# Kernel optimization log

Hardware: AMD Instinct MI355X
Metric: run time of the kernel (lower is better)

The kernel has to match this reference:

```python
import jax, jax.numpy as jnp
import numpy as np

COMMITMENT_COST = 0.25
EPS = 1e-10


def setup_inputs() -> dict:
    key = jax.random.key(0)
    k1, k2 = jax.random.split(key)
    z = jax.random.normal(k1, (8, 2048, 512), dtype=jnp.float32)
    # codebook ~ small uniform init in torch; small normal is fine for a numeric reference
    codebook = jax.random.normal(k2, (4096, 512), dtype=jnp.float32) * 0.02
    return {"z": z, "codebook": codebook}


def reference(z, codebook):
    B, S, D = z.shape
    K = codebook.shape[0]
    flat_z = z.reshape(-1, D)  # [N, D]
    distances = (
        jnp.sum(flat_z * flat_z, axis=1, keepdims=True)
        + jnp.sum(codebook * codebook, axis=1)
        - 2.0 * flat_z @ codebook.T
    )
    encoding_indices = jnp.argmin(distances, axis=1)  # [N] int
    z_q = codebook[encoding_indices].reshape(z.shape)  # gather lookup
    # commitment loss (z_q detached)
    commitment_loss = jnp.mean((z - jax.lax.stop_gradient(z_q)) ** 2)
    loss = COMMITMENT_COST * commitment_loss
    # straight-through estimator
    z_q_st = z + jax.lax.stop_gradient(z_q - z)
    # perplexity from codebook usage histogram
    N = flat_z.shape[0]
    counts = jnp.zeros((K,), dtype=jnp.float32).at[encoding_indices].add(1.0)
    avg_probs = counts / N
    perplexity = jnp.exp(-jnp.sum(avg_probs * jnp.log(avg_probs + EPS)))
    encoding_indices = encoding_indices.reshape(B, S)
    return (z_q_st, loss, encoding_indices, perplexity)
```

## Files before the change

### kernel.cpp

```cpp
#include <hip/hip_runtime.h>
#include <hip/hip_fp16.h>
#include <stdint.h>

#define B_  8
#define S_  2048
#define D_  512
#define K_  4096
#define N_  (B_ * S_)
#define NCB (K_ / 128)
#define NKB32 (D_ / 32)
#define MARGIN 0.014f

typedef _Float16 half8  __attribute__((ext_vector_type(8)));
typedef float    floatx4 __attribute__((ext_vector_type(4)));

#define OFF_PK   0
#define OFF_EN   (OFF_PK + (size_t)N_ * NCB * 8)
#define OFF_ZN   (OFF_EN + K_ * 4)
#define OFF_CNT  (OFF_ZN + N_ * 4)
#define OFF_BL   (OFF_CNT + K_ * 4)
#define OFF_ZH   (OFF_BL + 4096 * 4)
#define OFF_EH   (OFF_ZH + (size_t)N_ * D_ * 2)

__device__ __forceinline__ uint32_t umin32(uint32_t a, uint32_t b) { return a < b ? a : b; }
__device__ __forceinline__ uint32_t umax32(uint32_t a, uint32_t b) { return a > b ? a : b; }
__device__ __forceinline__ bool lexlt(float va, int ia, float vb, int ib) {
    return va < vb || (va == vb && ia < ib);
}

__device__ __forceinline__ void load_lds16(const _Float16* g, _Float16* l) {
    __builtin_amdgcn_global_load_lds(
        (const __attribute__((address_space(1))) unsigned int*)(uintptr_t)g,
        (__attribute__((address_space(3))) unsigned int*)(uintptr_t)l,
        16, 0, 0);
}

__global__ __launch_bounds__(256)
void vq_prep_kernel(const float* __restrict__ z, const float* __restrict__ cb,
                    _Float16* __restrict__ zh, _Float16* __restrict__ eh,
                    float* __restrict__ znorm, float* __restrict__ enorm,
                    int* __restrict__ counts) {
    const int t = threadIdx.x;
    if (blockIdx.x < 16) counts[blockIdx.x * 256 + t] = 0;

    const size_t u = (size_t)blockIdx.x * 256 + t;
    const int c   = (int)(u & 63);
    const int row = (int)(u >> 6);
    const bool isZ = row < N_;
    const int n = isZ ? row : row - N_;
    const float* r = (isZ ? z : cb) + (size_t)n * D_;

    float s = 0.f;
    for (int j = c; j < D_; j += 64) { float v = r[j]; s += v * v; }
    #pragma unroll
    for (int m = 1; m < 64; m <<= 1) s += __shfl_xor(s, m, 64);
    if (c == 0) { if (isZ) znorm[n] = s; else enorm[n] = s; }

    const float scale = isZ ? 1.0f : 64.0f;
    const float4 v0 = *(const float4*)(r + c * 8);
    const float4 v1 = *(const float4*)(r + c * 8 + 4);
    float a[8] = {v0.x, v0.y, v0.z, v0.w, v1.x, v1.y, v1.z, v1.w};
    half8 h;
    #pragma unroll
    for (int j = 0; j < 8; j++) h[j] = (_Float16)(a[j] * scale);
    const int kb = c >> 2, qd = c & 3;
    const int sw = qd ^ ((n >> 1) & 3);
    const size_t rows = isZ ? (size_t)N_ : (size_t)K_;
    const size_t off = (size_t)kb * rows * 32 + (size_t)n * 32 + (size_t)(sw << 3);
    *(half8*)((isZ ? zh : eh) + off) = h;
}

__global__ __launch_bounds__(256, 4)
void vq_dist_kernel(const _Float16* __restrict__ zh, const _Float16* __restrict__ eh,
                    const float* __restrict__ enorm, const float* __restrict__ znorm,
                    uint2* __restrict__ pK) {
    __shared__ _Float16 sA[2][4096];
    __shared__ float sE[128], sZn[128];
    __shared__ uint2 cK[2][128];

    const int t  = threadIdx.x;
    const int c0 = blockIdx.x * 128;
    const int m0 = blockIdx.y * 128;

    if (t < 128) { sE[t] = enorm[c0 + t]; sZn[t] = znorm[m0 + t]; }

    const int lane = t & 63, wid = t >> 6;
    const int wr = wid & 1, wc = wid >> 1;
    const int qd = lane >> 4, nl = lane & 15;
    const int sw8 = (qd ^ ((nl >> 1) & 3)) << 3;

    const _Float16* gsrc = zh + (size_t)m0 * 32 + (size_t)(wid * 2) * 512 + (size_t)lane * 8;
    const size_t strideA = (size_t)N_ * 32;
    const size_t strideB = (size_t)K_ * 32;
    const _Float16* bptr = eh + (size_t)c0 * 32 + (size_t)((wc * 64 + nl) * 32 + sw8);
    const int aoff = (wr * 64 + nl) * 32 + sw8;

    floatx4 acc[4][4];
    #pragma unroll
    for (int i = 0; i < 4; i++)
        #pragma unroll
        for (int j = 0; j < 4; j++) acc[i][j] = (floatx4)0.f;

    #pragma unroll
    for (int g = 0; g < 2; g++)
        load_lds16(gsrc + g * 512, sA[0] + wid * 2 * 512 + g * 512);

    for (int kb = 0; kb < NKB32; kb++) {
        __syncthreads();

        half8 b_h[4];
        #pragma unroll
        for (int s = 0; s < 4; s++)
            b_h[s] = *(const half8*)(bptr + s * 512);
        if (kb + 1 < NKB32) {
            const _Float16* gk = gsrc + (size_t)(kb + 1) * strideA;
            _Float16* ld = sA[(kb + 1) & 1] + wid * 2 * 512;
            #pragma unroll
            for (int g = 0; g < 2; g++)
                load_lds16(gk + g * 512, ld + g * 512);
        }
        const _Float16* ah = sA[kb & 1] + aoff;
        half8 a_h[4];
        #pragma unroll
        for (int s = 0; s < 4; s++)
            a_h[s] = *(const half8*)(ah + s * 512);
        #pragma unroll
        for (int i = 0; i < 4; i++)
            #pragma unroll
            for (int j = 0; j < 4; j++)
                acc[i][j] = __builtin_amdgcn_mfma_f32_16x16x32_f16(a_h[i], b_h[j], acc[i][j], 0, 0, 0);
        bptr += strideB;
    }

    uint32_t colc[4]; float se4[4];
    #pragma unroll
    for (int sn = 0; sn < 4; sn++) {
        const int cl = wc * 64 + sn * 16 + nl;
        colc[sn] = (uint32_t)cl;
        se4[sn]  = sE[cl];
    }
    #pragma unroll
    for (int sm = 0; sm < 4; sm++) {
        #pragma unroll
        for (int reg = 0; reg < 4; reg++) {
            const int rm = wr * 64 + sm * 16 + qd * 4 + reg;
            const float zn = sZn[rm];
            uint32_t k0 = 0xFFFFFFFFu, k1 = 0xFFFFFFFFu;
            #pragma unroll
            for (int sn = 0; sn < 4; sn++) {
                const float v = fmaf(acc[sm][sn][reg], -0.03125f, zn + se4[sn]);
                const uint32_t key = (__float_as_uint(v) & 0xFFFFFF80u) | colc[sn];
                const uint32_t t1 = umax32(k0, key);
                k1 = umin32(k1, t1);
                k0 = umin32(k0, key);
            }
            #pragma unroll
            for (int msk = 1; msk <= 8; msk <<= 1) {
                const uint32_t o0 = (uint32_t)__shfl_xor((int)k0, msk, 64);
                const uint32_t o1 = (uint32_t)__shfl_xor((int)k1, msk, 64);
                const uint32_t n0 = umin32(k0, o0);
                k1 = umin32(umax32(k0, o0), umin32(k1, o1));
                k0 = n0;
            }
            if (nl == 0) { cK[wc][rm].x = k0; cK[wc][rm].y = k1; }
        }
    }
    __syncthreads();
    if (t < 128) {
        const uint2 a = cK[0][t], b = cK[1][t];
        uint2 r;
        r.x = umin32(a.x, b.x);
        r.y = umin32(umax32(a.x, b.x), umin32(a.y, b.y));
        pK[(size_t)(m0 + t) * NCB + blockIdx.x] = r;
    }
}

__global__ __launch_bounds__(256)
void vq_gather_kernel(const float* __restrict__ z, const float* __restrict__ cb,
                      const float* __restrict__ znorm, const float* __restrict__ enorm,
                      const uint2* __restrict__ pK,
                      float* __restrict__ out_zq, float* __restrict__ out_idx,
                      int* __restrict__ counts, float* __restrict__ blockLoss) {
    const int lane = threadIdx.x & 63, wid = threadIdx.x >> 6;
    const int m = blockIdx.x * 4 + wid;

    uint32_t k0 = 0xFFFFFFFFu, k1 = 0xFFFFFFFFu;
    if (lane < NCB) {
        const uint2 kk = pK[(size_t)m * NCB + lane];
        k0 = kk.x; k1 = kk.y;
    }
    uint32_t g = k0;
    #pragma unroll
    for (int msk = 1; msk < 64; msk <<= 1) {
        const uint32_t o = (uint32_t)__shfl_xor((int)g, msk, 64);
        g = umin32(g, o);
    }
    const float gvf = __uint_as_float(g & 0xFFFFFF80u) + MARGIN;
    const bool f0 = (lane < NCB) && (__uint_as_float(k0 & 0xFFFFFF80u) <= gvf);
    const bool f1 = (lane < NCB) && (__uint_as_float(k1 & 0xFFFFFF80u) <= gvf);
    const unsigned long long b0 = __ballot(f0), b1 = __ballot(f1);
    int idx;
    if (__popcll(b0) + __popcll(b1) <= 1) {
        const unsigned long long bw = __ballot(k0 == g);
        idx = (int)__builtin_ctzll(bw) * 128 + (int)(g & 0x7Fu);
    } else {
        const float zn = znorm[m];
        const float* zrow = z + (size_t)m * D_;
        float bestd = 1e30f; int besti = 0x7fffffff;
        #pragma unroll
        for (int slot = 0; slot < 2; slot++) {
            unsigned long long bm = slot ? b1 : b0;
            while (bm) {
                const int l = (int)__builtin_ctzll(bm); bm &= bm - 1;
                const uint32_t kx = (uint32_t)__shfl((int)(slot ? k1 : k0), l, 64);
                const int cand = l * 128 + (int)(kx & 0x7Fu);
                const float* crow = cb + (size_t)cand * D_;
                float s = 0.f;
                #pragma unroll
                for (int j = 0; j < 8; j++)
                    s += zrow[lane * 8 + j] * crow[lane * 8 + j];
                #pragma unroll
                for (int msk = 1; msk < 64; msk <<= 1) s += __shfl_xor(s, msk, 64);
                const float d = (zn + enorm[cand]) - 2.0f * s;
                if (lexlt(d, cand, bestd, besti)) { bestd = d; besti = cand; }
            }
        }
        idx = besti;
    }

    const float4* qrow  = (const float4*)(cb + (size_t)idx * D_);
    const float4* zrow4 = (const float4*)(z + (size_t)m * D_);
    float4*       orow  = (float4*)(out_zq + (size_t)m * D_);
    float lsum = 0.f;
    #pragma unroll
    for (int i = 0; i < 2; i++) {
        const int j = lane + i * 64;
        const float4 q  = qrow[j];
        const float4 zv = zrow4[j];
        float4 o;
        o.x = zv.x + (q.x - zv.x); o.y = zv.y + (q.y - zv.y);
        o.z = zv.z + (q.z - zv.z); o.w = zv.w + (q.w - zv.w);
        orow[j] = o;
        const float dx = zv.x - q.x, dy = zv.y - q.y, dz = zv.z - q.z, dw = zv.w - q.w;
        lsum += dx * dx + dy * dy + dz * dz + dw * dw;
    }
    #pragma unroll
    for (int msk = 1; msk < 64; msk <<= 1) lsum += __shfl_xor(lsum, msk, 64);

    if (lane == 0) {
        out_idx[m] = (float)idx;
        atomicAdd(&counts[idx], 1);
    }
    __shared__ float wl[4];
    if (lane == 0) wl[wid] = lsum;
    __syncthreads();
    if (threadIdx.x == 0) blockLoss[blockIdx.x] = wl[0] + wl[1] + wl[2] + wl[3];
}

__global__ void vq_final_kernel(const int* __restrict__ counts,
                                const float* __restrict__ blockLoss,
                                float* __restrict__ out_loss, float* __restrict__ out_ppl) {
    __shared__ float sl[256], se[256];
    const int t = threadIdx.x;
    float ls = 0.f, es = 0.f;
    for (int i = t; i < N_ / 4; i += 256) ls += blockLoss[i];
    for (int k = t; k < K_; k += 256) {
        const float p = (float)counts[k] / (float)N_;
        es += p * logf(p + 1e-10f);
    }
    sl[t] = ls; se[t] = es;
    __syncthreads();
    for (int s = 128; s > 0; s >>= 1) {
        if (t < s) { sl[t] += sl[t + s]; se[t] += se[t + s]; }
        __syncthreads();
    }
    if (t == 0) {
        out_loss[0] = 0.25f * (sl[0] / (float)((size_t)N_ * D_));
        out_ppl[0]  = expf(-se[0]);
    }
}

extern "C" void kernel_launch(void* const* d_in, const int* in_sizes, int n_in,
                              void* d_out, int out_size, void* d_ws, size_t ws_size,
                              hipStream_t stream) {
    const float* z  = (const float*)d_in[0];
    const float* cb = (const float*)d_in[1];
    float* out = (float*)d_out;

    char* ws = (char*)d_ws;
    uint2*    pK        = (uint2*)   (ws + OFF_PK);
    float*    enorm     = (float*)   (ws + OFF_EN);
    float*    znorm     = (float*)   (ws + OFF_ZN);
    int*      counts    = (int*)     (ws + OFF_CNT);
    float*    blockLoss = (float*)   (ws + OFF_BL);
    _Float16* zh        = (_Float16*)(ws + OFF_ZH);
    _Float16* eh        = (_Float16*)(ws + OFF_EH);

    float* out_zq   = out;
    float* out_loss = out + (size_t)N_ * D_;
    float* out_idx  = out_loss + 1;
    float* out_ppl  = out_idx + N_;

    vq_prep_kernel<<<(N_ + K_) * 64 / 256, 256, 0, stream>>>(z, cb, zh, eh,
                                                             znorm, enorm, counts);

    dim3 grid(K_ / 128, N_ / 128);
    vq_dist_kernel<<<grid, 256, 0, stream>>>(zh, eh, enorm, znorm, pK);

    vq_gather_kernel<<<N_ / 4, 256, 0, stream>>>(z, cb, znorm, enorm, pK,
                                                 out_zq, out_idx, counts, blockLoss);

    vq_final_kernel<<<1, 256, 0, stream>>>(counts, blockLoss, out_loss, out_ppl);
}
```

Before: 205.2 us.

## Enlarge distance GEMM tile to 256x256 with 4-stage LDS pipeline for both operands

The distance kernel moves from 128x128 tiles with 256 threads to 256x256 tiles with 512 threads. Both the z and codebook fragments are now staged into LDS through a 4-deep ring of async global-to-LDS loads, using explicit vmcnt waits, raw barriers and MFMA priority boosts. Each wave computes 128x64 outputs in two half-steps, which raises reuse per loaded byte and overlaps loads with MFMA work. The cost is more registers and LDS per block, fewer blocks in the grid, and hand-tuned waitcnt logic that is fragile. The partial argmin output keeps its layout, written as two 128-column halves per block.

```diff
diff --git a/kernel.cpp b/kernel.cpp
--- a/kernel.cpp
+++ b/kernel.cpp
@@ -35,6 +35,9 @@
         16, 0, 0);
 }
 
+#define BARR() do { asm volatile("" ::: "memory"); __builtin_amdgcn_s_barrier(); \
+                    asm volatile("" ::: "memory"); } while (0)
+
 __global__ __launch_bounds__(256)
 void vq_prep_kernel(const float* __restrict__ z, const float* __restrict__ cb,
                     _Float16* __restrict__ zh, _Float16* __restrict__ eh,
@@ -70,84 +73,115 @@
     *(half8*)((isZ ? zh : eh) + off) = h;
 }
 
-__global__ __launch_bounds__(256, 4)
+__global__ __launch_bounds__(512, 2)
 void vq_dist_kernel(const _Float16* __restrict__ zh, const _Float16* __restrict__ eh,
                     const float* __restrict__ enorm, const float* __restrict__ znorm,
                     uint2* __restrict__ pK) {
-    __shared__ _Float16 sA[2][4096];
-    __shared__ float sE[128], sZn[128];
-    __shared__ uint2 cK[2][128];
+    __shared__ __align__(16) _Float16 sA[4][256 * 32];
+    __shared__ __align__(16) _Float16 sB[4][256 * 32];
 
     const int t  = threadIdx.x;
-    const int c0 = blockIdx.x * 128;
-    const int m0 = blockIdx.y * 128;
-
-    if (t < 128) { sE[t] = enorm[c0 + t]; sZn[t] = znorm[m0 + t]; }
-
+    const int c0 = blockIdx.x * 256;
+    const int m0 = blockIdx.y * 256;
     const int lane = t & 63, wid = t >> 6;
     const int wr = wid & 1, wc = wid >> 1;
     const int qd = lane >> 4, nl = lane & 15;
     const int sw8 = (qd ^ ((nl >> 1) & 3)) << 3;
 
-    const _Float16* gsrc = zh + (size_t)m0 * 32 + (size_t)(wid * 2) * 512 + (size_t)lane * 8;
     const size_t strideA = (size_t)N_ * 32;
     const size_t strideB = (size_t)K_ * 32;
-    const _Float16* bptr = eh + (size_t)c0 * 32 + (size_t)((wc * 64 + nl) * 32 + sw8);
-    const int aoff = (wr * 64 + nl) * 32 + sw8;
-
-    floatx4 acc[4][4];
-    #pragma unroll
-    for (int i = 0; i < 4; i++)
+    const _Float16* gA = zh + (size_t)m0 * 32;
+    const _Float16* gB = eh + (size_t)c0 * 32;
+    const size_t uo0 = (size_t)t * 8;
+    const size_t uo1 = (size_t)(512 + t) * 8;
+    const int lb0 = wid * 512;
+    const int lb1 = 4096 + wid * 512;
+
+    auto stageA = [&](int kb) {
+        const _Float16* g = gA + (size_t)kb * strideA;
+        _Float16* l = &sA[kb & 3][0];
+        load_lds16(g + uo0, l + lb0);
+        load_lds16(g + uo1, l + lb1);
+    };
+    auto stageB = [&](int kb) {
+        const _Float16* g = gB + (size_t)kb * strideB;
+        _Float16* l = &sB[kb & 3][0];
+        load_lds16(g + uo0, l + lb0);
+        load_lds16(g + uo1, l + lb1);
+    };
+
+    const int aBase = (wr * 128 + nl) * 32 + sw8;
+    const int bBase = (wc * 64 + nl) * 32 + sw8;
+
+    floatx4 acc[8][4];
+    #pragma unroll
+    for (int i = 0; i < 8; i++)
         #pragma unroll
         for (int j = 0; j < 4; j++) acc[i][j] = (floatx4)0.f;
 
-    #pragma unroll
-    for (int g = 0; g < 2; g++)
-        load_lds16(gsrc + g * 512, sA[0] + wid * 2 * 512 + g * 512);
-
-    for (int kb = 0; kb < NKB32; kb++) {
-        __syncthreads();
-
-        half8 b_h[4];
-        #pragma unroll
-        for (int s = 0; s < 4; s++)
-            b_h[s] = *(const half8*)(bptr + s * 512);
-        if (kb + 1 < NKB32) {
-            const _Float16* gk = gsrc + (size_t)(kb + 1) * strideA;
-            _Float16* ld = sA[(kb + 1) & 1] + wid * 2 * 512;
+    stageA(0); stageB(0);
+    stageA(1); stageB(1);
+    stageA(2); stageB(2);
+    asm volatile("s_waitcnt vmcnt(8)" ::: "memory");
+    BARR();
+
+    #pragma unroll
+    for (int s = 0; s < 16; ++s) {
+        const int slot = s & 3;
+        half8 b_h[4], a_h[4];
+        #pragma unroll
+        for (int j = 0; j < 4; ++j)
+            b_h[j] = *(const half8*)(&sB[slot][0] + bBase + j * 512);
+        #pragma unroll
+        for (int i = 0; i < 4; ++i)
+            a_h[i] = *(const half8*)(&sA[slot][0] + aBase + i * 512);
+        if (s < 13) stageA(s + 3);
+        BARR();
+        __builtin_amdgcn_s_setprio(1);
+        #pragma unroll
+        for (int i = 0; i < 4; ++i)
             #pragma unroll
-            for (int g = 0; g < 2; g++)
-                load_lds16(gk + g * 512, ld + g * 512);
-        }
-        const _Float16* ah = sA[kb & 1] + aoff;
-        half8 a_h[4];
-        #pragma unroll
-        for (int s = 0; s < 4; s++)
-            a_h[s] = *(const half8*)(ah + s * 512);
-        #pragma unroll
-        for (int i = 0; i < 4; i++)
+            for (int j = 0; j < 4; ++j)
+                acc[i][j] = __builtin_amdgcn_mfma_f32_16x16x32_f16(a_h[i], b_h[j], acc[i][j], 0, 0, 0);
+        __builtin_amdgcn_s_setprio(0);
+        BARR();
+        #pragma unroll
+        for (int i = 0; i < 4; ++i)
+            a_h[i] = *(const half8*)(&sA[slot][0] + aBase + 2048 + i * 512);
+        if (s < 13) stageB(s + 3);
+        BARR();
+        __builtin_amdgcn_s_setprio(1);
+        #pragma unroll
+        for (int i = 0; i < 4; ++i)
             #pragma unroll
-            for (int j = 0; j < 4; j++)
-                acc[i][j] = __builtin_amdgcn_mfma_f32_16x16x32_f16(a_h[i], b_h[j], acc[i][j], 0, 0, 0);
-        bptr += strideB;
-    }
+            for (int j = 0; j < 4; ++j)
+                acc[4 + i][j] = __builtin_amdgcn_mfma_f32_16x16x32_f16(a_h[i], b_h[j], acc[4 + i][j], 0, 0, 0);
+        __builtin_amdgcn_s_setprio(0);
+        if (s < 13)       { asm volatile("s_waitcnt vmcnt(8)" ::: "memory"); }
+        else if (s == 13) { asm volatile("s_waitcnt vmcnt(4)" ::: "memory"); }
+        else if (s == 14) { asm volatile("s_waitcnt vmcnt(0)" ::: "memory"); }
+        BARR();
+    }
+
+    uint2* cK = (uint2*)(&sA[0][0]);
 
     uint32_t colc[4]; float se4[4];
-    #pragma unroll
-    for (int sn = 0; sn < 4; sn++) {
-        const int cl = wc * 64 + sn * 16 + nl;
+    const int colbase = (wc & 1) * 64;
+    #pragma unroll
+    for (int sn = 0; sn < 4; ++sn) {
+        const int cl = colbase + sn * 16 + nl;
         colc[sn] = (uint32_t)cl;
-        se4[sn]  = sE[cl];
-    }
-    #pragma unroll
-    for (int sm = 0; sm < 4; sm++) {
-        #pragma unroll
-        for (int reg = 0; reg < 4; reg++) {
-            const int rm = wr * 64 + sm * 16 + qd * 4 + reg;
-            const float zn = sZn[rm];
+        se4[sn]  = enorm[c0 + wc * 64 + sn * 16 + nl];
+    }
+    #pragma unroll
+    for (int sm = 0; sm < 8; ++sm) {
+        #pragma unroll
+        for (int reg = 0; reg < 4; ++reg) {
+            const int rm = wr * 128 + sm * 16 + qd * 4 + reg;
+            const float zn = znorm[m0 + rm];
             uint32_t k0 = 0xFFFFFFFFu, k1 = 0xFFFFFFFFu;
             #pragma unroll
-            for (int sn = 0; sn < 4; sn++) {
+            for (int sn = 0; sn < 4; ++sn) {
                 const float v = fmaf(acc[sm][sn][reg], -0.03125f, zn + se4[sn]);
                 const uint32_t key = (__float_as_uint(v) & 0xFFFFFF80u) | colc[sn];
                 const uint32_t t1 = umax32(k0, key);
@@ -162,16 +196,18 @@
                 k1 = umin32(umax32(k0, o0), umin32(k1, o1));
                 k0 = n0;
             }
-            if (nl == 0) { cK[wc][rm].x = k0; cK[wc][rm].y = k1; }
+            if (nl == 0) { cK[wc * 256 + rm].x = k0; cK[wc * 256 + rm].y = k1; }
         }
     }
     __syncthreads();
-    if (t < 128) {
-        const uint2 a = cK[0][t], b = cK[1][t];
+    {
+        const int row = t & 255, b = t >> 8;
+        const uint2 a = cK[(b * 2) * 256 + row];
+        const uint2 c = cK[(b * 2 + 1) * 256 + row];
         uint2 r;
-        r.x = umin32(a.x, b.x);
-        r.y = umin32(umax32(a.x, b.x), umin32(a.y, b.y));
-        pK[(size_t)(m0 + t) * NCB + blockIdx.x] = r;
+        r.x = umin32(a.x, c.x);
+        r.y = umin32(umax32(a.x, c.x), umin32(a.y, c.y));
+        pK[(size_t)(m0 + row) * NCB + blockIdx.x * 2 + b] = r;
     }
 }
 
@@ -304,8 +340,8 @@
     vq_prep_kernel<<<(N_ + K_) * 64 / 256, 256, 0, stream>>>(z, cb, zh, eh,
                                                              znorm, enorm, counts);
 
-    dim3 grid(K_ / 128, N_ / 128);
-    vq_dist_kernel<<<grid, 256, 0, stream>>>(zh, eh, enorm, znorm, pK);
+    dim3 grid(K_ / 256, N_ / 256);
+    vq_dist_kernel<<<grid, 512, 0, stream>>>(zh, eh, enorm, znorm, pK);
 
     vq_gather_kernel<<<N_ / 4, 256, 0, stream>>>(z, cb, znorm, enorm, pK,
                                                  out_zq, out_idx, counts, blockLoss);
```

Result: slower. 217.3 us (+5.9%).

## Stage codebook tiles through LDS and fold final reduction into gather kernel

Applied to the files above, without the earlier changes.

The distance GEMM now loads the codebook (B) tile into double-buffered LDS with async global-to-LDS copies alongside the z tile, instead of each wave reading B fragments straight from global memory. The separate single-block final kernel is removed. The last gather block to finish, found with an atomic done-counter and thread fences, computes the loss and perplexity. This cuts redundant global traffic for B and one kernel launch, at the cost of twice the LDS per block, which may reduce occupancy, and an extra atomic in every gather block.

```diff
diff --git a/kernel.cpp b/kernel.cpp
--- a/kernel.cpp
+++ b/kernel.cpp
@@ -19,7 +19,8 @@
 #define OFF_ZN   (OFF_EN + K_ * 4)
 #define OFF_CNT  (OFF_ZN + N_ * 4)
 #define OFF_BL   (OFF_CNT + K_ * 4)
-#define OFF_ZH   (OFF_BL + 4096 * 4)
+#define OFF_DC   (OFF_BL + 4096 * 4)
+#define OFF_ZH   (OFF_DC + 64)
 #define OFF_EH   (OFF_ZH + (size_t)N_ * D_ * 2)
 
 __device__ __forceinline__ uint32_t umin32(uint32_t a, uint32_t b) { return a < b ? a : b; }
@@ -39,9 +40,10 @@
 void vq_prep_kernel(const float* __restrict__ z, const float* __restrict__ cb,
                     _Float16* __restrict__ zh, _Float16* __restrict__ eh,
                     float* __restrict__ znorm, float* __restrict__ enorm,
-                    int* __restrict__ counts) {
+                    int* __restrict__ counts, int* __restrict__ doneCnt) {
     const int t = threadIdx.x;
     if (blockIdx.x < 16) counts[blockIdx.x * 256 + t] = 0;
+    if (blockIdx.x == 16 && t == 0) doneCnt[0] = 0;
 
     const size_t u = (size_t)blockIdx.x * 256 + t;
     const int c   = (int)(u & 63);
@@ -74,7 +76,8 @@
 void vq_dist_kernel(const _Float16* __restrict__ zh, const _Float16* __restrict__ eh,
                     const float* __restrict__ enorm, const float* __restrict__ znorm,
                     uint2* __restrict__ pK) {
-    __shared__ _Float16 sA[2][4096];
+    __shared__ __align__(16) _Float16 sA[2][4096];
+    __shared__ __align__(16) _Float16 sB[2][4096];
     __shared__ float sE[128], sZn[128];
     __shared__ uint2 cK[2][128];
 
@@ -89,11 +92,13 @@
     const int qd = lane >> 4, nl = lane & 15;
     const int sw8 = (qd ^ ((nl >> 1) & 3)) << 3;
 
-    const _Float16* gsrc = zh + (size_t)m0 * 32 + (size_t)(wid * 2) * 512 + (size_t)lane * 8;
     const size_t strideA = (size_t)N_ * 32;
     const size_t strideB = (size_t)K_ * 32;
-    const _Float16* bptr = eh + (size_t)c0 * 32 + (size_t)((wc * 64 + nl) * 32 + sw8);
+    const _Float16* gA = zh + (size_t)m0 * 32 + (size_t)t * 8;
+    const _Float16* gB = eh + (size_t)c0 * 32 + (size_t)t * 8;
+
     const int aoff = (wr * 64 + nl) * 32 + sw8;
+    const int boff = (wc * 64 + nl) * 32 + sw8;
 
     floatx4 acc[4][4];
     #pragma unroll
@@ -101,24 +106,28 @@
         #pragma unroll
         for (int j = 0; j < 4; j++) acc[i][j] = (floatx4)0.f;
 
-    #pragma unroll
-    for (int g = 0; g < 2; g++)
-        load_lds16(gsrc + g * 512, sA[0] + wid * 2 * 512 + g * 512);
+    auto stage = [&](int kb) {
+        const _Float16* ga = gA + (size_t)kb * strideA;
+        const _Float16* gb = gB + (size_t)kb * strideB;
+        _Float16* la = sA[kb & 1] + t * 8;
+        _Float16* lb = sB[kb & 1] + t * 8;
+        load_lds16(ga, la);
+        load_lds16(ga + 2048, la + 2048);
+        load_lds16(gb, lb);
+        load_lds16(gb + 2048, lb + 2048);
+    };
+
+    stage(0);
 
     for (int kb = 0; kb < NKB32; kb++) {
         __syncthreads();
-
+        if (kb + 1 < NKB32) stage(kb + 1);
+
+        const _Float16* bh = sB[kb & 1] + boff;
         half8 b_h[4];
         #pragma unroll
         for (int s = 0; s < 4; s++)
-            b_h[s] = *(const half8*)(bptr + s * 512);
-        if (kb + 1 < NKB32) {
-            const _Float16* gk = gsrc + (size_t)(kb + 1) * strideA;
-            _Float16* ld = sA[(kb + 1) & 1] + wid * 2 * 512;
-            #pragma unroll
-            for (int g = 0; g < 2; g++)
-                load_lds16(gk + g * 512, ld + g * 512);
-        }
+            b_h[s] = *(const half8*)(bh + s * 512);
         const _Float16* ah = sA[kb & 1] + aoff;
         half8 a_h[4];
         #pragma unroll
@@ -129,7 +138,6 @@
             #pragma unroll
             for (int j = 0; j < 4; j++)
                 acc[i][j] = __builtin_amdgcn_mfma_f32_16x16x32_f16(a_h[i], b_h[j], acc[i][j], 0, 0, 0);
-        bptr += strideB;
     }
 
     uint32_t colc[4]; float se4[4];
@@ -180,7 +188,9 @@
                       const float* __restrict__ znorm, const float* __restrict__ enorm,
                       const uint2* __restrict__ pK,
                       float* __restrict__ out_zq, float* __restrict__ out_idx,
-                      int* __restrict__ counts, float* __restrict__ blockLoss) {
+                      int* __restrict__ counts, float* __restrict__ blockLoss,
+                      int* __restrict__ doneCnt,
+                      float* __restrict__ out_loss, float* __restrict__ out_ppl) {
     const int lane = threadIdx.x & 63, wid = threadIdx.x >> 6;
     const int m = blockIdx.x * 4 + wid;
 
@@ -255,28 +265,31 @@
     if (lane == 0) wl[wid] = lsum;
     __syncthreads();
     if (threadIdx.x == 0) blockLoss[blockIdx.x] = wl[0] + wl[1] + wl[2] + wl[3];
-}
-
-__global__ void vq_final_kernel(const int* __restrict__ counts,
-                                const float* __restrict__ blockLoss,
-                                float* __restrict__ out_loss, float* __restrict__ out_ppl) {
-    __shared__ float sl[256], se[256];
-    const int t = threadIdx.x;
-    float ls = 0.f, es = 0.f;
-    for (int i = t; i < N_ / 4; i += 256) ls += blockLoss[i];
-    for (int k = t; k < K_; k += 256) {
-        const float p = (float)counts[k] / (float)N_;
-        es += p * logf(p + 1e-10f);
-    }
-    sl[t] = ls; se[t] = es;
+
+    __shared__ int sLast;
+    __threadfence();
+    if (threadIdx.x == 0) sLast = (atomicAdd(doneCnt, 1) == (N_ / 4) - 1) ? 1 : 0;
     __syncthreads();
-    for (int s = 128; s > 0; s >>= 1) {
-        if (t < s) { sl[t] += sl[t + s]; se[t] += se[t + s]; }
+    if (sLast) {
+        __threadfence();
+        __shared__ float sl[256], se[256];
+        const int tt = threadIdx.x;
+        float ls = 0.f, es = 0.f;
+        for (int i = tt; i < N_ / 4; i += 256) ls += blockLoss[i];
+        for (int k = tt; k < K_; k += 256) {
+            const float p = (float)counts[k] / (float)N_;
+            es += p * logf(p + 1e-10f);
+        }
+        sl[tt] = ls; se[tt] = es;
         __syncthreads();
-    }
-    if (t == 0) {
-        out_loss[0] = 0.25f * (sl[0] / (float)((size_t)N_ * D_));
-        out_ppl[0]  = expf(-se[0]);
+        for (int s = 128; s > 0; s >>= 1) {
+            if (tt < s) { sl[tt] += sl[tt + s]; se[tt] += se[tt + s]; }
+            __syncthreads();
+        }
+        if (tt == 0) {
+            out_loss[0] = 0.25f * (sl[0] / (float)((size_t)N_ * D_));
+            out_ppl[0]  = expf(-se[0]);
+        }
     }
 }
 
@@ -293,6 +306,7 @@
     float*    znorm     = (float*)   (ws + OFF_ZN);
     int*      counts    = (int*)     (ws + OFF_CNT);
     float*    blockLoss = (float*)   (ws + OFF_BL);
+    int*      doneCnt   = (int*)     (ws + OFF_DC);
     _Float16* zh        = (_Float16*)(ws + OFF_ZH);
     _Float16* eh        = (_Float16*)(ws + OFF_EH);
 
@@ -302,13 +316,12 @@
     float* out_ppl  = out_idx + N_;
 
     vq_prep_kernel<<<(N_ + K_) * 64 / 256, 256, 0, stream>>>(z, cb, zh, eh,
-                                                             znorm, enorm, counts);
+                                                             znorm, enorm, counts, doneCnt);
 
     dim3 grid(K_ / 128, N_ / 128);
     vq_dist_kernel<<<grid, 256, 0, stream>>>(zh, eh, enorm, znorm, pK);
 
     vq_gather_kernel<<<N_ / 4, 256, 0, stream>>>(z, cb, znorm, enorm, pK,
-                                                 out_zq, out_idx, counts, blockLoss);
-
-    vq_final_kernel<<<1, 256, 0, stream>>>(counts, blockLoss, out_loss, out_ppl);
-}
+                                                 out_zq, out_idx, counts, blockLoss,
+                                                 doneCnt, out_loss, out_ppl);
+}
```

Measured after the change: 703.8 us. +243.0%, slower.

## Give each wave a private LDS A tile with two-stage prefetch and no block barriers

Applied to the files above, without the earlier changes.

Each wave now stages its own 64-row A slice into a private double-buffered LDS region, prefetching two k-steps ahead. The per-iteration __syncthreads is replaced by explicit vmcnt/lgkmcnt waits, removing block-wide synchronization from the main loop. The cost is duplicated A loads across the two waves that share a row half, plus twice the LDS footprint. Correctness now depends on the hand-coded wait counts matching the number of outstanding loads.

```diff
diff --git a/kernel.cpp b/kernel.cpp
--- a/kernel.cpp
+++ b/kernel.cpp
@@ -74,7 +74,7 @@
 void vq_dist_kernel(const _Float16* __restrict__ zh, const _Float16* __restrict__ eh,
                     const float* __restrict__ enorm, const float* __restrict__ znorm,
                     uint2* __restrict__ pK) {
-    __shared__ _Float16 sA[2][4096];
+    __shared__ __align__(16) _Float16 sAw[4][2][2048];
     __shared__ float sE[128], sZn[128];
     __shared__ uint2 cK[2][128];
 
@@ -89,11 +89,11 @@
     const int qd = lane >> 4, nl = lane & 15;
     const int sw8 = (qd ^ ((nl >> 1) & 3)) << 3;
 
-    const _Float16* gsrc = zh + (size_t)m0 * 32 + (size_t)(wid * 2) * 512 + (size_t)lane * 8;
     const size_t strideA = (size_t)N_ * 32;
     const size_t strideB = (size_t)K_ * 32;
+    const _Float16* gA = zh + (size_t)(m0 + wr * 64) * 32 + (size_t)lane * 8;
     const _Float16* bptr = eh + (size_t)c0 * 32 + (size_t)((wc * 64 + nl) * 32 + sw8);
-    const int aoff = (wr * 64 + nl) * 32 + sw8;
+    const int aoff = nl * 32 + sw8;
 
     floatx4 acc[4][4];
     #pragma unroll
@@ -101,36 +101,44 @@
         #pragma unroll
         for (int j = 0; j < 4; j++) acc[i][j] = (floatx4)0.f;
 
-    #pragma unroll
-    for (int g = 0; g < 2; g++)
-        load_lds16(gsrc + g * 512, sA[0] + wid * 2 * 512 + g * 512);
-
+    auto stage = [&](int kb) {
+        const _Float16* g = gA + (size_t)kb * strideA;
+        _Float16* l = &sAw[wid][kb & 1][0];
+        #pragma unroll
+        for (int i = 0; i < 4; i++)
+            load_lds16(g + i * 512, l + i * 512);
+    };
+
+    stage(0);
+    stage(1);
+
+    #pragma unroll 1
     for (int kb = 0; kb < NKB32; kb++) {
-        __syncthreads();
-
-        half8 b_h[4];
-        #pragma unroll
-        for (int s = 0; s < 4; s++)
-            b_h[s] = *(const half8*)(bptr + s * 512);
-        if (kb + 1 < NKB32) {
-            const _Float16* gk = gsrc + (size_t)(kb + 1) * strideA;
-            _Float16* ld = sA[(kb + 1) & 1] + wid * 2 * 512;
-            #pragma unroll
-            for (int g = 0; g < 2; g++)
-                load_lds16(gk + g * 512, ld + g * 512);
-        }
-        const _Float16* ah = sA[kb & 1] + aoff;
+        if (kb == 0) asm volatile("s_waitcnt vmcnt(4)" ::: "memory");
+        else         asm volatile("s_waitcnt vmcnt(8)" ::: "memory");
+
+        const _Float16* ah = &sAw[wid][kb & 1][0] + aoff;
         half8 a_h[4];
         #pragma unroll
         for (int s = 0; s < 4; s++)
             a_h[s] = *(const half8*)(ah + s * 512);
+        asm volatile("s_waitcnt lgkmcnt(0)" ::: "memory");
+        __builtin_amdgcn_sched_barrier(0);
+        if (kb + 2 < NKB32) stage(kb + 2);
+
+        const _Float16* bp = bptr + (size_t)kb * strideB;
+        half8 b_h[4];
+        #pragma unroll
+        for (int s = 0; s < 4; s++)
+            b_h[s] = *(const half8*)(bp + s * 512);
         #pragma unroll
         for (int i = 0; i < 4; i++)
             #pragma unroll
             for (int j = 0; j < 4; j++)
                 acc[i][j] = __builtin_amdgcn_mfma_f32_16x16x32_f16(a_h[i], b_h[j], acc[i][j], 0, 0, 0);
-        bptr += strideB;
-    }
+    }
+
+    __syncthreads();
 
     uint32_t colc[4]; float se4[4];
     #pragma unroll
```

Result: slower. 210.4 us (+2.5%).
